# Optimization experiments

Hardware: AMD Instinct MI355X
Metric: run time of the kernel (lower is better)

Reference implementation:

```python
import jax, jax.numpy as jnp
import numpy as np

N, H, T, B = 64, 8, 256, 16
S, K = 4, 16          # num_segments, topk_edges_per_seg
EPS = 1e-8
TOTAL = S * (N * 9 + K * 4)  # 2560


def setup_inputs() -> dict:
    key = jax.random.key(0)
    ks = jax.random.split(key, 4)
    return {
        "sat_scores_seq": jax.random.normal(ks[0], (B, T, H, N, N), dtype=jnp.float32),
        "ln_gamma": jnp.ones((TOTAL,), dtype=jnp.float32),
        "ln_beta": jnp.zeros((TOTAL,), dtype=jnp.float32),
        "W1": jax.random.normal(ks[1], (TOTAL, 128), dtype=jnp.float32) * 0.02,
        "b1": jnp.zeros((128,), dtype=jnp.float32),
        "W2": jax.random.normal(ks[2], (128, 64), dtype=jnp.float32) * 0.02,
        "b2": jnp.zeros((64,), dtype=jnp.float32),
    }


def reference(sat_scores_seq, ln_gamma, ln_beta, W1, b1, W2, b2):
    b, t, h, n, _ = sat_scores_seq.shape
    L = t // S  # equal-length segments (t divisible by S)
    P = jax.nn.softmax(sat_scores_seq, axis=-1)          # [B,T,H,N,N]
    Ph = P.mean(axis=2)                                  # head-avg [B,T,N,N]
    Ps = Ph.reshape(b, S, L, n, n)                       # [B,S,L,N,N]

    # --- node features (all stats over segment time dim) ---
    Pc = jnp.maximum(Ps, EPS)
    ent = -(jnp.log(Pc) * Pc).sum(axis=-1)               # [B,S,L,N]
    ent_mean = ent.mean(axis=2)
    ent_std = ent.std(axis=2, ddof=1)
    ent_range = ent.max(axis=2) - ent.min(axis=2)
    ent_slope = (ent[:, :, -1] - ent[:, :, 0]) / max(L - 1, 1)
    diag = jnp.diagonal(Ps, axis1=-2, axis2=-1)          # [B,S,L,N]
    diag_mean = diag.mean(axis=2)
    diag_std = diag.std(axis=2, ddof=1)
    dPs = Ps[:, :, 1:] - Ps[:, :, :-1]                   # [B,S,L-1,N,N]
    diff = jnp.abs(dPs).sum(axis=-1)                     # [B,S,L-1,N]
    var_mean = diff.mean(axis=2)
    var_std = diff.std(axis=2, ddof=1)
    var_max = diff.max(axis=2)
    node = jnp.stack([ent_mean, ent_std, ent_range, ent_slope,
                      var_mean, var_std, var_max, diag_mean, diag_std],
                     axis=-1)                            # [B,S,N,9]
    node = node.reshape(b, S, n * 9)

    # --- edge features + top-k selection ---
    P_edge_mean = Ps.mean(axis=2)                        # [B,S,N,N]
    dP_mean = dPs.mean(axis=2)
    dP_std = dPs.std(axis=2, ddof=1)
    edge = jnp.stack([P_edge_mean, dP_std,
                      jax.nn.relu(dP_mean), jax.nn.relu(-dP_mean)],
                     axis=-1).reshape(b, S, n * n, 4)    # [B,S,N*N,4]
    score = jnp.abs(dP_mean).reshape(b, S, n * n)
    diag_idx = jnp.arange(0, n * n, n + 1)
    score = score.at[:, :, diag_idx].set(0.0)            # exclude self-edges
    k = min(K, n * n - n)
    _, idx = jax.lax.top_k(score, k)                     # [B,S,k]
    topk_feat = jnp.take_along_axis(edge, idx[..., None], axis=2)  # [B,S,k,4]

    feat = jnp.concatenate([node, topk_feat.reshape(b, S, k * 4)],
                           axis=-1).reshape(b, -1)       # [B, S*(9N+4k)]

    # --- projection head: LayerNorm -> Linear -> ReLU -> Linear -> ReLU ---
    mu = feat.mean(axis=-1, keepdims=True)
    var = feat.var(axis=-1, keepdims=True)
    hfeat = (feat - mu) * jax.lax.rsqrt(var + 1e-5) * ln_gamma + ln_beta
    hfeat = jax.nn.relu(hfeat @ W1 + b1)
    return jax.nn.relu(hfeat @ W2 + b2)                  # [B, out_dim]
```

## Files before the change

kernel.cpp:

```cpp
#include <hip/hip_runtime.h>
#include <hip/hip_bf16.h>
#include <math.h>

#define EPSV 1e-8f

typedef float floatx4 __attribute__((ext_vector_type(4)));

template <int CTRL, bool ZERO>
__device__ __forceinline__ float fdpp(float v) {
  return __int_as_float(__builtin_amdgcn_update_dpp(
      ZERO ? 0 : __float_as_int(v), __float_as_int(v), CTRL, 0xF, 0xF, ZERO));
}
__device__ __forceinline__ float rdl63(float v) {
  return __int_as_float(__builtin_amdgcn_readlane(__float_as_int(v), 63));
}
__device__ __forceinline__ float gsum8(float v) {
  v += fdpp<0xB1, true>(v);
  v += fdpp<0x4E, true>(v);
  v += fdpp<0x141, true>(v);
  return v;
}
__device__ __forceinline__ float gmax8(float v) {
  v = fmaxf(v, fdpp<0xB1, false>(v));
  v = fmaxf(v, fdpp<0x4E, false>(v));
  v = fmaxf(v, fdpp<0x141, false>(v));
  return v;
}
__device__ __forceinline__ float wsum_dpp(float v) {
  v += fdpp<0x111, true>(v);
  v += fdpp<0x112, true>(v);
  v += fdpp<0x114, true>(v);
  v += fdpp<0x118, true>(v);
  v += fdpp<0x142, true>(v);
  v += fdpp<0x143, true>(v);
  return rdl63(v);
}
__device__ __forceinline__ float wmax_dpp(float v) {
  v = fmaxf(v, fdpp<0x111, false>(v));
  v = fmaxf(v, fdpp<0x112, false>(v));
  v = fmaxf(v, fdpp<0x114, false>(v));
  v = fmaxf(v, fdpp<0x118, false>(v));
  v = fmaxf(v, fdpp<0x142, false>(v));
  v = fmaxf(v, fdpp<0x143, false>(v));
  return rdl63(v);
}
__device__ __forceinline__ float wmin_dpp(float v) {
  v = fminf(v, fdpp<0x111, false>(v));
  v = fminf(v, fdpp<0x112, false>(v));
  v = fminf(v, fdpp<0x114, false>(v));
  v = fminf(v, fdpp<0x118, false>(v));
  v = fminf(v, fdpp<0x142, false>(v));
  v = fminf(v, fdpp<0x143, false>(v));
  return rdl63(v);
}

__device__ __forceinline__ float wsum64(float v) {
#pragma unroll
  for (int m = 1; m <= 32; m <<= 1) v += __shfl_xor(v, m);
  return v;
}

__device__ __forceinline__ floatx4 ntload4(const float* p) {
  return __builtin_nontemporal_load((const floatx4*)p);
}

__global__ __launch_bounds__(512, 8) void stage1_kernel(
    const float* __restrict__ sat, float* __restrict__ node,
    float* __restrict__ edge, float* __restrict__ score) {
  const int bid = blockIdx.x;
  const int n = bid & 63;
  const int bs = bid >> 6;
  const int tbase = bs * 64;

  __shared__ float Ps[64][64];
  __shared__ float ent_s[64];
  __shared__ float diff_s[64];
  __shared__ float psum_s[8][64];
  __shared__ float dsq_s[8][64];

  const int tid = threadIdx.x;
  const int wave = tid >> 6;
  const int lane = tid & 63;
  const int rsub = lane >> 3;
  const int sl = lane & 7;
  const int l = wave * 8 + rsub;

  const float* rowb =
      sat + (size_t)(tbase + l) * 32768 + n * 64 + sl * 4;

  float acc[8];
#pragma unroll
  for (int c = 0; c < 8; ++c) acc[c] = 0.f;

#pragma unroll 4
  for (int h = 0; h < 8; ++h) {
    const float* p = rowb + h * 4096;
    floatx4 r0 = ntload4(p);
    floatx4 r1 = ntload4(p + 32);
    float m = fmaxf(fmaxf(fmaxf(r0.x, r0.y), fmaxf(r0.z, r0.w)),
                    fmaxf(fmaxf(r1.x, r1.y), fmaxf(r1.z, r1.w)));
    m = gmax8(m);
    float e0 = __expf(r0.x - m), e1 = __expf(r0.y - m);
    float e2 = __expf(r0.z - m), e3 = __expf(r0.w - m);
    float e4 = __expf(r1.x - m), e5 = __expf(r1.y - m);
    float e6 = __expf(r1.z - m), e7 = __expf(r1.w - m);
    float s = gsum8(((e0 + e1) + (e2 + e3)) + ((e4 + e5) + (e6 + e7)));
    float inv = 1.0f / s;
    acc[0] += e0 * inv; acc[1] += e1 * inv;
    acc[2] += e2 * inv; acc[3] += e3 * inv;
    acc[4] += e4 * inv; acc[5] += e5 * inv;
    acc[6] += e6 * inv; acc[7] += e7 * inv;
  }

  float ent = 0.f;
#pragma unroll
  for (int c = 0; c < 8; ++c) {
    acc[c] *= 0.125f;
    float pc = fmaxf(acc[c], EPSV);
    ent += pc * __logf(pc);
  }
  ent = gsum8(ent);
  if (sl == 0) ent_s[l] = -ent;

  *(float4*)&Ps[l][sl * 4] = *(float4*)&acc[0];
  *(float4*)&Ps[l][sl * 4 + 32] = *(float4*)&acc[4];
  __syncthreads();

  {
    const int base = wave * 8;
    float psum = 0.f, dsq = 0.f;
    float p = Ps[base][lane];
#pragma unroll 1
    for (int i = 0; i < 8; ++i) {
      const int ll = base + i;
      psum += p;
      if (ll < 63) {
        float pn = Ps[ll + 1][lane];
        float d = pn - p;
        dsq += d * d;
        float ad = fabsf(d);
        ad += fdpp<0x111, true>(ad);
        ad += fdpp<0x112, true>(ad);
        ad += fdpp<0x114, true>(ad);
        ad += fdpp<0x118, true>(ad);
        ad += fdpp<0x142, true>(ad);
        ad += fdpp<0x143, true>(ad);
        if (lane == 63) diff_s[ll] = ad;
        p = pn;
      }
    }
    psum_s[wave][lane] = psum;
    dsq_s[wave][lane] = dsq;
  }
  __syncthreads();

  if (wave == 1) {
    const int j = lane;
    float tot = 0.f, dsq = 0.f;
#pragma unroll
    for (int w = 0; w < 8; ++w) {
      tot += psum_s[w][j];
      dsq += dsq_s[w][j];
    }
    float pem = tot * (1.0f / 64.0f);
    float dmean = (Ps[63][j] - Ps[0][j]) * (1.0f / 63.0f);
    float dvar = (dsq - 63.0f * dmean * dmean) * (1.0f / 62.0f);
    float dstd = sqrtf(fmaxf(dvar, 0.f));
    size_t eo = (size_t)bs * 4096 + (size_t)n * 64 + j;
    float4 ef = make_float4(pem, dstd, fmaxf(dmean, 0.f), fmaxf(-dmean, 0.f));
    *(float4*)(edge + eo * 4) = ef;
    score[eo] = (j == n) ? 0.f : fabsf(dmean);
  }

  if (wave == 0) {
    float e = ent_s[lane];
    float dg = Ps[lane][n];
    bool dv = lane < 63;
    float df = dv ? diff_s[lane] : 0.f;

    float emean = wsum_dpp(e) * (1.0f / 64.0f);
    float emax = wmax_dpp(e);
    float emin = wmin_dpp(e);
    float dgmean = wsum_dpp(dg) * (1.0f / 64.0f);
    float dfmean = wsum_dpp(df) * (1.0f / 63.0f);
    float dfmax = wmax_dpp(dv ? df : -INFINITY);

    float ed = e - emean;
    float evar = wsum_dpp(ed * ed) * (1.0f / 63.0f);
    float dgd = dg - dgmean;
    float dgvar = wsum_dpp(dgd * dgd) * (1.0f / 63.0f);
    float dfd = dv ? (df - dfmean) : 0.f;
    float dfvar = wsum_dpp(dfd * dfd) * (1.0f / 62.0f);

    if (lane == 0) {
      float* no = node + ((size_t)bs * 64 + n) * 9;
      no[0] = emean;
      no[1] = sqrtf(fmaxf(evar, 0.f));
      no[2] = emax - emin;
      no[3] = (ent_s[63] - ent_s[0]) * (1.0f / 63.0f);
      no[4] = dfmean;
      no[5] = sqrtf(fmaxf(dfvar, 0.f));
      no[6] = dfmax;
      no[7] = dgmean;
      no[8] = sqrtf(fmaxf(dgvar, 0.f));
    }
  }
}

__global__ __launch_bounds__(256) void stage2_kernel(
    const float* __restrict__ node, const float* __restrict__ edge,
    const float* __restrict__ score, float* __restrict__ feat) {
  const int bsid = blockIdx.x;
  const int b = bsid >> 2, s = bsid & 3;
  __shared__ float sc[4096];
  __shared__ int widx[16];
  __shared__ float rv[4];
  __shared__ int ri[4];
  const int tid = threadIdx.x;
  const int wave = tid >> 6, lane = tid & 63;

  const float* scg = score + (size_t)bsid * 4096;
  for (int i = tid; i < 4096; i += 256) sc[i] = scg[i];
  __syncthreads();

  for (int k = 0; k < 16; ++k) {
    float bv = -1.f;
    int bi = 1 << 30;
    for (int i = tid; i < 4096; i += 256) {
      float v = sc[i];
      if (v > bv) { bv = v; bi = i; }
    }
#pragma unroll
    for (int mk = 1; mk <= 32; mk <<= 1) {
      float ov = __shfl_xor(bv, mk);
      int oi = __shfl_xor(bi, mk);
      if (ov > bv || (ov == bv && oi < bi)) { bv = ov; bi = oi; }
    }
    if (lane == 0) { rv[wave] = bv; ri[wave] = bi; }
    __syncthreads();
    if (tid == 0) {
      float fv = rv[0]; int fi = ri[0];
#pragma unroll
      for (int w = 1; w < 4; ++w)
        if (rv[w] > fv || (rv[w] == fv && ri[w] < fi)) { fv = rv[w]; fi = ri[w]; }
      widx[k] = fi;
      sc[fi] = -1.f;
    }
    __syncthreads();
  }

  float* fout = feat + (size_t)b * 2560 + s * 640;
  const float* nodeg = node + (size_t)bsid * 576;
  for (int i = tid; i < 576; i += 256) fout[i] = nodeg[i];
  if (tid < 16) {
    int idx = widx[tid];
    float4 ef = *(const float4*)(edge + ((size_t)bsid * 4096 + idx) * 4);
    *(float4*)(fout + 576 + tid * 4) = ef;
  }
}

__global__ __launch_bounds__(256) void stage3_kernel(
    const float* __restrict__ feat, const float* __restrict__ gamma,
    const float* __restrict__ beta, const float* __restrict__ W1,
    const float* __restrict__ b1, const float* __restrict__ W2,
    const float* __restrict__ b2, float* __restrict__ out) {
  const int b = blockIdx.x;
  __shared__ float hf[2560];
  __shared__ float rs[4], rq[4];
  __shared__ float part[2][128];
  __shared__ float h1[128];
  __shared__ float part2[4][64];
  const int tid = threadIdx.x;
  const int wave = tid >> 6, lane = tid & 63;

  const float* f = feat + (size_t)b * 2560;
  float lsum = 0.f, lsq = 0.f;
  for (int i = tid; i < 2560; i += 256) {
    float v = f[i];
    hf[i] = v;
    lsum += v;
    lsq += v * v;
  }
  lsum = wsum64(lsum);
  lsq = wsum64(lsq);
  if (lane == 0) { rs[wave] = lsum; rq[wave] = lsq; }
  __syncthreads();
  float tsum = rs[0] + rs[1] + rs[2] + rs[3];
  float tsq = rq[0] + rq[1] + rq[2] + rq[3];
  float mean = tsum * (1.0f / 2560.0f);
  float var = tsq * (1.0f / 2560.0f) - mean * mean;
  float inv = rsqrtf(var + 1e-5f);
  for (int i = tid; i < 2560; i += 256)
    hf[i] = (hf[i] - mean) * inv * gamma[i] + beta[i];
  __syncthreads();

  {
    const int o = tid & 127, half = tid >> 7;
    float acc = 0.f;
    const int i0 = half * 1280;
    for (int i = i0; i < i0 + 1280; ++i) acc += hf[i] * W1[(size_t)i * 128 + o];
    part[half][o] = acc;
  }
  __syncthreads();
  if (tid < 128) h1[tid] = fmaxf(part[0][tid] + part[1][tid] + b1[tid], 0.f);
  __syncthreads();
  {
    const int o = tid & 63, pp = tid >> 6;
    float acc = 0.f;
    const int i0 = pp * 32;
    for (int i = i0; i < i0 + 32; ++i) acc += h1[i] * W2[i * 64 + o];
    part2[pp][o] = acc;
  }
  __syncthreads();
  if (tid < 64)
    out[(size_t)b * 64 + tid] =
        fmaxf(part2[0][tid] + part2[1][tid] + part2[2][tid] + part2[3][tid] + b2[tid], 0.f);
}

extern "C" void kernel_launch(void* const* d_in, const int* in_sizes, int n_in,
                              void* d_out, int out_size, void* d_ws, size_t ws_size,
                              hipStream_t stream) {
  const float* sat = (const float*)d_in[0];
  const float* gamma = (const float*)d_in[1];
  const float* beta = (const float*)d_in[2];
  const float* W1 = (const float*)d_in[3];
  const float* b1 = (const float*)d_in[4];
  const float* W2 = (const float*)d_in[5];
  const float* b2 = (const float*)d_in[6];
  float* out = (float*)d_out;

  float* ws = (float*)d_ws;
  float* edge = ws;
  float* score = edge + 16 * 4 * 4096 * 4;
  float* node = score + 16 * 4 * 4096;
  float* feat = node + 16 * 4 * 64 * 9;

  stage1_kernel<<<4096, 512, 0, stream>>>(sat, node, edge, score);
  stage2_kernel<<<64, 256, 0, stream>>>(node, edge, score, feat);
  stage3_kernel<<<16, 256, 0, stream>>>(feat, gamma, beta, W1, b1, W2, b2, out);
}
```

Measured before the change: 151.2 us.

## Split fused softmax/stats kernel into contiguous softmax pass plus stats pass

```diff
diff --git a/kernel.cpp b/kernel.cpp
--- a/kernel.cpp
+++ b/kernel.cpp
@@ -64,8 +64,54 @@
   return __builtin_nontemporal_load((const floatx4*)p);
 }
 
-__global__ __launch_bounds__(512, 8) void stage1_kernel(
-    const float* __restrict__ sat, float* __restrict__ node,
+__global__ __launch_bounds__(256, 8) void softmax_kernel(
+    const float* __restrict__ sat, float* __restrict__ pst) {
+  const int bid = blockIdx.x;
+  const int tid = threadIdx.x;
+  const int sl = tid & 7;
+  const int grp = tid >> 3;
+
+  const float* base = sat + (size_t)bid * 32768;
+  float* outb = pst + (size_t)bid * 4096;
+
+#pragma unroll 1
+  for (int half = 0; half < 2; ++half) {
+    const int n = grp + half * 32;
+    const float* rowb = base + n * 64 + sl * 4;
+
+    float acc[8];
+#pragma unroll
+    for (int c = 0; c < 8; ++c) acc[c] = 0.f;
+
+#pragma unroll 4
+    for (int h = 0; h < 8; ++h) {
+      const float* p = rowb + h * 4096;
+      floatx4 r0 = ntload4(p);
+      floatx4 r1 = ntload4(p + 32);
+      float m = fmaxf(fmaxf(fmaxf(r0.x, r0.y), fmaxf(r0.z, r0.w)),
+                      fmaxf(fmaxf(r1.x, r1.y), fmaxf(r1.z, r1.w)));
+      m = gmax8(m);
+      float e0 = __expf(r0.x - m), e1 = __expf(r0.y - m);
+      float e2 = __expf(r0.z - m), e3 = __expf(r0.w - m);
+      float e4 = __expf(r1.x - m), e5 = __expf(r1.y - m);
+      float e6 = __expf(r1.z - m), e7 = __expf(r1.w - m);
+      float s = gsum8(((e0 + e1) + (e2 + e3)) + ((e4 + e5) + (e6 + e7)));
+      float inv = 1.0f / s;
+      acc[0] += e0 * inv; acc[1] += e1 * inv;
+      acc[2] += e2 * inv; acc[3] += e3 * inv;
+      acc[4] += e4 * inv; acc[5] += e5 * inv;
+      acc[6] += e6 * inv; acc[7] += e7 * inv;
+    }
+
+#pragma unroll
+    for (int c = 0; c < 8; ++c) acc[c] *= 0.125f;
+    *(float4*)(outb + n * 64 + sl * 4) = *(float4*)&acc[0];
+    *(float4*)(outb + n * 64 + sl * 4 + 32) = *(float4*)&acc[4];
+  }
+}
+
+__global__ __launch_bounds__(256, 4) void stats_kernel(
+    const float* __restrict__ pst, float* __restrict__ node,
     float* __restrict__ edge, float* __restrict__ score) {
   const int bid = blockIdx.x;
   const int n = bid & 63;
@@ -75,64 +121,39 @@
   __shared__ float Ps[64][64];
   __shared__ float ent_s[64];
   __shared__ float diff_s[64];
-  __shared__ float psum_s[8][64];
-  __shared__ float dsq_s[8][64];
+  __shared__ float psum_s[4][64];
+  __shared__ float dsq_s[4][64];
 
   const int tid = threadIdx.x;
   const int wave = tid >> 6;
   const int lane = tid & 63;
-  const int rsub = lane >> 3;
-  const int sl = lane & 7;
-  const int l = wave * 8 + rsub;
-
-  const float* rowb =
-      sat + (size_t)(tbase + l) * 32768 + n * 64 + sl * 4;
-
-  float acc[8];
-#pragma unroll
-  for (int c = 0; c < 8; ++c) acc[c] = 0.f;
-
-#pragma unroll 4
-  for (int h = 0; h < 8; ++h) {
-    const float* p = rowb + h * 4096;
-    floatx4 r0 = ntload4(p);
-    floatx4 r1 = ntload4(p + 32);
-    float m = fmaxf(fmaxf(fmaxf(r0.x, r0.y), fmaxf(r0.z, r0.w)),
-                    fmaxf(fmaxf(r1.x, r1.y), fmaxf(r1.z, r1.w)));
-    m = gmax8(m);
-    float e0 = __expf(r0.x - m), e1 = __expf(r0.y - m);
-    float e2 = __expf(r0.z - m), e3 = __expf(r0.w - m);
-    float e4 = __expf(r1.x - m), e5 = __expf(r1.y - m);
-    float e6 = __expf(r1.z - m), e7 = __expf(r1.w - m);
-    float s = gsum8(((e0 + e1) + (e2 + e3)) + ((e4 + e5) + (e6 + e7)));
-    float inv = 1.0f / s;
-    acc[0] += e0 * inv; acc[1] += e1 * inv;
-    acc[2] += e2 * inv; acc[3] += e3 * inv;
-    acc[4] += e4 * inv; acc[5] += e5 * inv;
-    acc[6] += e6 * inv; acc[7] += e7 * inv;
-  }
-
-  float ent = 0.f;
-#pragma unroll
-  for (int c = 0; c < 8; ++c) {
-    acc[c] *= 0.125f;
-    float pc = fmaxf(acc[c], EPSV);
-    ent += pc * __logf(pc);
-  }
-  ent = gsum8(ent);
-  if (sl == 0) ent_s[l] = -ent;
-
-  *(float4*)&Ps[l][sl * 4] = *(float4*)&acc[0];
-  *(float4*)&Ps[l][sl * 4 + 32] = *(float4*)&acc[4];
+
+#pragma unroll
+  for (int i = 0; i < 4; ++i) {
+    const int idx = i * 256 + tid;
+    const int row = idx >> 4;
+    const int c4 = idx & 15;
+    *(float4*)&Ps[row][c4 * 4] =
+        *(const float4*)(pst + ((size_t)(tbase + row) * 64 + n) * 64 + c4 * 4);
+  }
   __syncthreads();
 
   {
-    const int base = wave * 8;
+    const int base = wave * 16;
     float psum = 0.f, dsq = 0.f;
     float p = Ps[base][lane];
 #pragma unroll 1
-    for (int i = 0; i < 8; ++i) {
+    for (int i = 0; i < 16; ++i) {
       const int ll = base + i;
+      float pc = fmaxf(p, EPSV);
+      float e = pc * __logf(pc);
+      e += fdpp<0x111, true>(e);
+      e += fdpp<0x112, true>(e);
+      e += fdpp<0x114, true>(e);
+      e += fdpp<0x118, true>(e);
+      e += fdpp<0x142, true>(e);
+      e += fdpp<0x143, true>(e);
+      if (lane == 63) ent_s[ll] = -e;
       psum += p;
       if (ll < 63) {
         float pn = Ps[ll + 1][lane];
@@ -156,12 +177,8 @@
 
   if (wave == 1) {
     const int j = lane;
-    float tot = 0.f, dsq = 0.f;
-#pragma unroll
-    for (int w = 0; w < 8; ++w) {
-      tot += psum_s[w][j];
-      dsq += dsq_s[w][j];
-    }
+    float tot = psum_s[0][j] + psum_s[1][j] + psum_s[2][j] + psum_s[3][j];
+    float dsq = dsq_s[0][j] + dsq_s[1][j] + dsq_s[2][j] + dsq_s[3][j];
     float pem = tot * (1.0f / 64.0f);
     float dmean = (Ps[63][j] - Ps[0][j]) * (1.0f / 63.0f);
     float dvar = (dsq - 63.0f * dmean * dmean) * (1.0f / 62.0f);
@@ -330,12 +347,14 @@
   float* out = (float*)d_out;
 
   float* ws = (float*)d_ws;
-  float* edge = ws;
+  float* pst = ws;
+  float* edge = pst + 16777216;
   float* score = edge + 16 * 4 * 4096 * 4;
   float* node = score + 16 * 4 * 4096;
   float* feat = node + 16 * 4 * 64 * 9;
 
-  stage1_kernel<<<4096, 512, 0, stream>>>(sat, node, edge, score);
+  softmax_kernel<<<4096, 256, 0, stream>>>(sat, pst);
+  stats_kernel<<<4096, 256, 0, stream>>>(pst, node, edge, score);
   stage2_kernel<<<64, 256, 0, stream>>>(node, edge, score, feat);
   stage3_kernel<<<16, 256, 0, stream>>>(feat, gamma, beta, W1, b1, W2, b2, out);
 }
```

Measured after the change: 202.7 us. 34.1% more time.

## Stream head slices into LDS via async global_load_lds triple buffering

Applied to the files above, without the earlier changes.

```diff
diff --git a/kernel.cpp b/kernel.cpp
--- a/kernel.cpp
+++ b/kernel.cpp
@@ -60,11 +60,7 @@
   return v;
 }
 
-__device__ __forceinline__ floatx4 ntload4(const float* p) {
-  return __builtin_nontemporal_load((const floatx4*)p);
-}
-
-__global__ __launch_bounds__(512, 8) void stage1_kernel(
+__global__ __launch_bounds__(512, 6) void stage1_kernel(
     const float* __restrict__ sat, float* __restrict__ node,
     float* __restrict__ edge, float* __restrict__ score) {
   const int bid = blockIdx.x;
@@ -72,31 +68,57 @@
   const int bs = bid >> 6;
   const int tbase = bs * 64;
 
-  __shared__ float Ps[64][64];
+  __shared__ float buf[3][64][64];
   __shared__ float ent_s[64];
   __shared__ float diff_s[64];
   __shared__ float psum_s[8][64];
   __shared__ float dsq_s[8][64];
+  float (*Ps)[64] = buf[0];
 
   const int tid = threadIdx.x;
   const int wave = tid >> 6;
   const int lane = tid & 63;
-  const int rsub = lane >> 3;
-  const int sl = lane & 7;
-  const int l = wave * 8 + rsub;
-
-  const float* rowb =
-      sat + (size_t)(tbase + l) * 32768 + n * 64 + sl * 4;
+  const int grp_l = tid >> 3;
+  const int sl = tid & 7;
+  const int w8 = wave * 8;
+
+  const float* sat_w = sat + (size_t)(tbase + w8) * 32768 + n * 64;
+
+  auto stage = [&](int h) {
+    const int d = h % 3;
+    const float* g0 =
+        sat_w + (size_t)h * 4096 + (size_t)(lane >> 4) * 32768 + (lane & 15) * 4;
+    __builtin_amdgcn_global_load_lds(
+        (const __attribute__((address_space(1))) void*)g0,
+        (__attribute__((address_space(3))) void*)&buf[d][w8][0], 16, 0, 2);
+    const float* g1 = g0 + 4ull * 32768;
+    __builtin_amdgcn_global_load_lds(
+        (const __attribute__((address_space(1))) void*)g1,
+        (__attribute__((address_space(3))) void*)&buf[d][w8 + 4][0], 16, 0, 2);
+  };
+
+  stage(0);
+  stage(1);
+  stage(2);
 
   float acc[8];
 #pragma unroll
   for (int c = 0; c < 8; ++c) acc[c] = 0.f;
 
-#pragma unroll 4
+#pragma unroll
   for (int h = 0; h < 8; ++h) {
-    const float* p = rowb + h * 4096;
-    floatx4 r0 = ntload4(p);
-    floatx4 r1 = ntload4(p + 32);
+    if (h <= 5) {
+      asm volatile("s_waitcnt vmcnt(4)" ::: "memory");
+    } else if (h == 6) {
+      asm volatile("s_waitcnt vmcnt(2)" ::: "memory");
+    } else {
+      asm volatile("s_waitcnt vmcnt(0)" ::: "memory");
+    }
+    __builtin_amdgcn_sched_barrier(0);
+
+    float4 r0 = *(const float4*)&buf[h % 3][grp_l][sl * 4];
+    float4 r1 = *(const float4*)&buf[h % 3][grp_l][sl * 4 + 32];
+
     float m = fmaxf(fmaxf(fmaxf(r0.x, r0.y), fmaxf(r0.z, r0.w)),
                     fmaxf(fmaxf(r1.x, r1.y), fmaxf(r1.z, r1.w)));
     m = gmax8(m);
@@ -110,6 +132,8 @@
     acc[2] += e2 * inv; acc[3] += e3 * inv;
     acc[4] += e4 * inv; acc[5] += e5 * inv;
     acc[6] += e6 * inv; acc[7] += e7 * inv;
+
+    if (h + 3 < 8) stage(h + 3);
   }
 
   float ent = 0.f;
@@ -120,10 +144,10 @@
     ent += pc * __logf(pc);
   }
   ent = gsum8(ent);
-  if (sl == 0) ent_s[l] = -ent;
-
-  *(float4*)&Ps[l][sl * 4] = *(float4*)&acc[0];
-  *(float4*)&Ps[l][sl * 4 + 32] = *(float4*)&acc[4];
+  if (sl == 0) ent_s[grp_l] = -ent;
+
+  *(float4*)&Ps[grp_l][sl * 4] = *(float4*)&acc[0];
+  *(float4*)&Ps[grp_l][sl * 4 + 32] = *(float4*)&acc[4];
   __syncthreads();
 
   {
```

After: 180.7 us. 19.5% more time.
